# Kernel optimization log

Measured on AMD Instinct MI355X. Metric: run time of the kernel, lower is better.

Reference implementation:

```python
import jax, jax.numpy as jnp
import numpy as np

T, B, H = 512, 128, 512


def setup_inputs() -> dict:
    key = jax.random.key(0)
    k1, k2, k3 = jax.random.split(key, 3)
    x = jax.random.normal(k1, (T, B, H), dtype=jnp.float32)
    h0 = jnp.zeros((B, H), dtype=jnp.float32)
    # Orthogonal-ish scale via normal/sqrt(H) to keep gates in sane range
    Wi = jax.random.normal(k2, (H, 3 * H), dtype=jnp.float32) / np.sqrt(H)
    bi = jnp.zeros((3 * H,), dtype=jnp.float32)
    Wh = jax.random.normal(k3, (H, 3 * H), dtype=jnp.float32) / np.sqrt(H)
    bhn = jnp.zeros((H,), dtype=jnp.float32)
    return {"x": x, "h0": h0, "Wi": Wi, "bi": bi, "Wh": Wh, "bhn": bhn}


def reference(x, h0, Wi, bi, Wh, bhn):
    """GRU scanned over time, matching flax nn.GRUCell math.

    x: [T, B, H]; h0: [B, H]; Wi: [H, 3H] (r|z|n), bi: [3H];
    Wh: [H, 3H] (r|z|n, no bias except n-gate bhn: [H]).
    Returns (final_carry [B,H], outputs [T,B,H]).
    """
    hdim = h0.shape[-1]
    # Precompute all input projections in one big GEMM: [T, B, 3H]
    gi = jnp.einsum('tbh,hk->tbk', x, Wi) + bi

    def step(h, gi_t):
        gh = h @ Wh  # [B, 3H]
        gi_r, gi_z, gi_n = jnp.split(gi_t, 3, axis=-1)
        gh_r, gh_z, gh_n = jnp.split(gh, 3, axis=-1)
        r = jax.nn.sigmoid(gi_r + gh_r)
        z = jax.nn.sigmoid(gi_z + gh_z)
        n = jnp.tanh(gi_n + r * (gh_n + bhn))
        h_new = (1.0 - z) * n + z * h
        return h_new, h_new

    h_final, ys = jax.lax.scan(step, h0, gi)
    return h_final, ys
```

## Files before the change

kernel.cpp:

```cpp
#include <hip/hip_runtime.h>


#define TT 512
#define BB 128
#define HH 512
#define H3 1536
#define NWG 256
#define NTHR 1024

#define LDS_FLOATS 31232

__global__ __launch_bounds__(NTHR)
__attribute__((amdgpu_waves_per_eu(4, 4)))
void gru_scan(
    const float* __restrict__ x,
    const float* __restrict__ h0,
    const float* __restrict__ Wi,
    const float* __restrict__ bi,
    const float* __restrict__ Wh,
    const float* __restrict__ bhn,
    float* out,
    unsigned int* __restrict__ bars)
{
  __shared__ float lds[LDS_FLOATS];
  float*  Xs   = lds;
  float*  Hs   = lds + 8192;
  float4* red  = reinterpret_cast<float4*>(lds + 16384);
  float*  sums = lds + 29696;

  const int tid = threadIdx.x;
  const int n   = blockIdx.x;
  const int jt  = n & 31;
  const int bt  = n >> 5;
  const int j0  = jt * 16;
  const int b0  = bt * 16;

  const int w   = tid >> 6;
  const int kg  = (tid >> 4) & 3;
  const int jl  = tid & 15;
  const int kbase = (w & 7) * 64;
  const bool isH = (w < 8);

  unsigned int* grp = bars + bt * 32;

  float wa[48];
  {
    const float* __restrict__ W = isH ? Wh : Wi;
    #pragma unroll
    for (int m = 0; m < 4; ++m)
      #pragma unroll
      for (int kk = 0; kk < 4; ++kk) {
        const int k = kbase + m * 16 + kg * 4 + kk;
        #pragma unroll
        for (int g = 0; g < 3; ++g) {
          const float v = W[(size_t)k * H3 + g * HH + j0 + jl];
          asm volatile("v_accvgpr_write_b32 %0, %1"
                       : "=a"(wa[(m * 4 + kk) * 3 + g]) : "v"(v));
        }
      }
  }

  float* ys = out + BB * HH;

  float bir = 0.f, biz = 0.f, bin = 0.f, bhnv = 0.f;
  if (tid < 256) {
    const int jj = j0 + (tid & 15);
    bir  = bi[jj];
    biz  = bi[jj + HH];
    bin  = bi[jj + 2 * HH];
    bhnv = bhn[jj];
  }

  for (int t = 0; t < TT; ++t) {
    const float* __restrict__ xt = x + (size_t)t * BB * HH;
    const float* hp = t ? (ys + (size_t)(t - 1) * BB * HH) : h0;

    #pragma unroll
    for (int i = 0; i < 8; ++i) {
      const int idx = tid + i * NTHR;
      const int r = idx >> 9;
      const int c = idx & 511;
      Hs[r * 512 + c] = __hip_atomic_load(
          const_cast<float*>(hp) + (size_t)(b0 + r) * HH + c,
          __ATOMIC_RELAXED, __HIP_MEMORY_SCOPE_AGENT);
    }
    #pragma unroll
    for (int i = 0; i < 2; ++i) {
      const int idx = tid + i * NTHR;
      const int r = idx >> 7;
      const int c = idx & 127;
      const float4 xv = ((const float4*)(xt + (size_t)(b0 + r) * HH))[c];
      *(float4*)&Xs[r * 512 + c * 4] = xv;
    }
    __syncthreads();

    {
      const float* __restrict__ S = isH ? Hs : Xs;
      #pragma unroll
      for (int bq = 0; bq < 4; ++bq) {
        float a[4][3];
        #pragma unroll
        for (int r = 0; r < 4; ++r)
          #pragma unroll
          for (int g = 0; g < 3; ++g) a[r][g] = 0.f;

        #pragma unroll
        for (int m = 0; m < 4; ++m) {
          float wv[12];
          #pragma unroll
          for (int kk = 0; kk < 4; ++kk)
            #pragma unroll
            for (int g = 0; g < 3; ++g)
              asm volatile("v_accvgpr_read_b32 %0, %1"
                           : "=v"(wv[kk * 3 + g])
                           : "a"(wa[(m * 4 + kk) * 3 + g]));

          const float* Sm = S + kbase + m * 16 + kg * 4;
          const float4 v0 = *(const float4*)(Sm + (bq * 4 + 0) * 512);
          const float4 v1 = *(const float4*)(Sm + (bq * 4 + 1) * 512);
          const float4 v2 = *(const float4*)(Sm + (bq * 4 + 2) * 512);
          const float4 v3 = *(const float4*)(Sm + (bq * 4 + 3) * 512);
          #pragma unroll
          for (int g = 0; g < 3; ++g) {
            a[0][g] += v0.x*wv[0+g] + v0.y*wv[3+g] + v0.z*wv[6+g] + v0.w*wv[9+g];
            a[1][g] += v1.x*wv[0+g] + v1.y*wv[3+g] + v1.z*wv[6+g] + v1.w*wv[9+g];
            a[2][g] += v2.x*wv[0+g] + v2.y*wv[3+g] + v2.z*wv[6+g] + v2.w*wv[9+g];
            a[3][g] += v3.x*wv[0+g] + v3.y*wv[3+g] + v3.z*wv[6+g] + v3.w*wv[9+g];
          }
        }

        #pragma unroll
        for (int r = 0; r < 4; ++r)
          #pragma unroll
          for (int g = 0; g < 3; ++g) {
            a[r][g] += __shfl_xor(a[r][g], 16);
            a[r][g] += __shfl_xor(a[r][g], 32);
          }

        if (kg == bq) {
          float4* rp = red + (size_t)(w * 16 + jl) * 13 + bq * 3;
          #pragma unroll
          for (int g = 0; g < 3; ++g)
            rp[g] = make_float4(a[0][g], a[1][g], a[2][g], a[3][g]);
        }
      }
    }

    if (t + 1 < TT) {
      const float* xn = x + (size_t)(t + 1) * BB * HH;
      #pragma unroll
      for (int i = 0; i < 2; ++i) {
        const int idx = tid + i * NTHR;
        const int r = idx >> 7;
        const int c = idx & 127;
        const float4 v = ((const float4*)(xn + (size_t)(b0 + r) * HH))[c];
        asm volatile("" :: "v"(v.x), "v"(v.y), "v"(v.z), "v"(v.w));
      }
    }
    __syncthreads();

    {
      const int pm = tid >> 9;
      const int t9 = tid & 511;
      const int pjl = (t9 >> 4) & 15;
      const int pg  = (t9 >> 2) & 3;
      const int pbq = t9 & 3;
      if ((t9 & 256) == 0 && pg < 3) {
        float4 s = make_float4(0.f, 0.f, 0.f, 0.f);
        #pragma unroll
        for (int w2 = 0; w2 < 8; ++w2) {
          const float4 v = red[(size_t)(pm * 128 + w2 * 16 + pjl) * 13 + pbq * 3 + pg];
          s.x += v.x; s.y += v.y; s.z += v.z; s.w += v.w;
        }
        *(float4*)&sums[(size_t)(((pm * 16 + pjl) * 3) + pg) * 16 + pbq * 4] = s;
      }
    }
    __syncthreads();

    if (tid < 256) {
      const int eb  = tid >> 4;
      const int jl2 = tid & 15;
      const int jj  = j0 + jl2;
      const float ghr = sums[(jl2*3 + 0)*16 + eb];
      const float ghz = sums[(jl2*3 + 1)*16 + eb];
      const float ghn = sums[(jl2*3 + 2)*16 + eb];
      const float gir = sums[((16 + jl2)*3 + 0)*16 + eb];
      const float giz = sums[((16 + jl2)*3 + 1)*16 + eb];
      const float gin = sums[((16 + jl2)*3 + 2)*16 + eb];

      const float gr = gir + ghr + bir;
      const float gz = giz + ghz + biz;
      const float r  = 1.f / (1.f + __expf(-gr));
      const float z  = 1.f / (1.f + __expf(-gz));
      const float pre = gin + bin + r * (ghn + bhnv);
      const float e2 = __expf(2.f * pre);
      const float nn = 1.f - 2.f / (e2 + 1.f);
      const float hpv = Hs[eb * 512 + jj];
      const float h = (1.f - z) * nn + z * hpv;

      const size_t o = (size_t)(b0 + eb) * HH + jj;
      __hip_atomic_store(ys + (size_t)t * BB * HH + o, h,
                         __ATOMIC_RELAXED, __HIP_MEMORY_SCOPE_AGENT);
      if (t == TT - 1) out[o] = h;
    }

    if (t + 1 < TT) {
      __syncthreads();
      if (tid == 0) {
        __hip_atomic_fetch_add(grp, 1u, __ATOMIC_RELEASE,
                               __HIP_MEMORY_SCOPE_AGENT);
        const unsigned int target = 32u * (unsigned int)(t + 1);
        while (__hip_atomic_load(grp, __ATOMIC_RELAXED,
                                 __HIP_MEMORY_SCOPE_AGENT) < target)
          __builtin_amdgcn_s_sleep(1);
      }
      __syncthreads();
    }
  }
}

extern "C" void kernel_launch(void* const* d_in, const int* in_sizes, int n_in,
                              void* d_out, int out_size, void* d_ws, size_t ws_size,
                              hipStream_t stream) {
  const float* x   = (const float*)d_in[0];
  const float* h0  = (const float*)d_in[1];
  const float* Wi  = (const float*)d_in[2];
  const float* bi  = (const float*)d_in[3];
  const float* Wh  = (const float*)d_in[4];
  const float* bhn = (const float*)d_in[5];
  float* out = (float*)d_out;
  unsigned int* bars = (unsigned int*)d_ws;

  hipMemsetAsync(d_ws, 0, 8 * 128, stream);

  void* args[] = {(void*)&x, (void*)&h0, (void*)&Wi, (void*)&bi,
                  (void*)&Wh, (void*)&bhn, (void*)&out, (void*)&bars};
  hipLaunchCooperativeKernel(reinterpret_cast<const void*>(gru_scan),
                             dim3(NWG), dim3(NTHR), args, 0, stream);
}
```

Measured before the change: 15.74 ms.

## Split batch tile into two half-groups with separate barriers to overlap sync

```diff
diff --git a/kernel.cpp b/kernel.cpp
--- a/kernel.cpp
+++ b/kernel.cpp
@@ -8,7 +8,9 @@
 #define NWG 256
 #define NTHR 1024
 
-#define LDS_FLOATS 31232
+#define LDS_FLOATS 24320
+
+typedef float f32x4_t __attribute__((ext_vector_type(4)));
 
 __global__ __launch_bounds__(NTHR)
 __attribute__((amdgpu_waves_per_eu(4, 4)))
@@ -23,17 +25,20 @@
     unsigned int* __restrict__ bars)
 {
   __shared__ float lds[LDS_FLOATS];
-  float*  Xs   = lds;
-  float*  Hs   = lds + 8192;
+  float*  XsA  = lds;
+  float*  XsB  = lds + 4096;
+  float*  HsA  = lds + 8192;
+  float*  HsB  = lds + 12288;
   float4* red  = reinterpret_cast<float4*>(lds + 16384);
-  float*  sums = lds + 29696;
+  float*  sums = lds + 23552;
 
   const int tid = threadIdx.x;
   const int n   = blockIdx.x;
   const int jt  = n & 31;
-  const int bt  = n >> 5;
   const int j0  = jt * 16;
-  const int b0  = bt * 16;
+  const int btA = n >> 5;
+  const int b0A = btA * 8;
+  const int b0B = b0A + 64;
 
   const int w   = tid >> 6;
   const int kg  = (tid >> 4) & 3;
@@ -41,7 +46,8 @@
   const int kbase = (w & 7) * 64;
   const bool isH = (w < 8);
 
-  unsigned int* grp = bars + bt * 32;
+  unsigned int* grpA = bars + btA * 32;
+  unsigned int* grpB = bars + (btA + 8) * 32;
 
   float wa[48];
   {
@@ -63,7 +69,7 @@
   float* ys = out + BB * HH;
 
   float bir = 0.f, biz = 0.f, bin = 0.f, bhnv = 0.f;
-  if (tid < 256) {
+  if (tid < 128) {
     const int jj = j0 + (tid & 15);
     bir  = bi[jj];
     biz  = bi[jj + HH];
@@ -71,148 +77,163 @@
     bhnv = bhn[jj];
   }
 
+  {
+    const int r = tid >> 7;
+    const int c = tid & 127;
+    *(float4*)&XsA[r * 512 + c * 4] = ((const float4*)(x  + (size_t)(b0A + r) * HH))[c];
+    *(float4*)&XsB[r * 512 + c * 4] = ((const float4*)(x  + (size_t)(b0B + r) * HH))[c];
+    *(float4*)&HsA[r * 512 + c * 4] = ((const float4*)(h0 + (size_t)(b0A + r) * HH))[c];
+    *(float4*)&HsB[r * 512 + c * 4] = ((const float4*)(h0 + (size_t)(b0B + r) * HH))[c];
+  }
+  __syncthreads();
+
   for (int t = 0; t < TT; ++t) {
-    const float* __restrict__ xt = x + (size_t)t * BB * HH;
-    const float* hp = t ? (ys + (size_t)(t - 1) * BB * HH) : h0;
-
     #pragma unroll
-    for (int i = 0; i < 8; ++i) {
-      const int idx = tid + i * NTHR;
-      const int r = idx >> 9;
-      const int c = idx & 511;
-      Hs[r * 512 + c] = __hip_atomic_load(
-          const_cast<float*>(hp) + (size_t)(b0 + r) * HH + c,
-          __ATOMIC_RELAXED, __HIP_MEMORY_SCOPE_AGENT);
-    }
-    #pragma unroll
-    for (int i = 0; i < 2; ++i) {
-      const int idx = tid + i * NTHR;
-      const int r = idx >> 7;
-      const int c = idx & 127;
-      const float4 xv = ((const float4*)(xt + (size_t)(b0 + r) * HH))[c];
-      *(float4*)&Xs[r * 512 + c * 4] = xv;
-    }
-    __syncthreads();
-
-    {
-      const float* __restrict__ S = isH ? Hs : Xs;
-      #pragma unroll
-      for (int bq = 0; bq < 4; ++bq) {
-        float a[4][3];
+    for (int ph = 0; ph < 2; ++ph) {
+      const float* Hsx = ph ? HsB : HsA;
+      const float* Xsx = ph ? XsB : XsA;
+      const int    b0  = ph ? b0B : b0A;
+
+      {
+        const float* __restrict__ S = (isH ? Hsx : Xsx) + kbase;
         #pragma unroll
-        for (int r = 0; r < 4; ++r)
-          #pragma unroll
-          for (int g = 0; g < 3; ++g) a[r][g] = 0.f;
-
-        #pragma unroll
-        for (int m = 0; m < 4; ++m) {
-          float wv[12];
-          #pragma unroll
-          for (int kk = 0; kk < 4; ++kk)
+        for (int q = 0; q < 2; ++q) {
+          float a[4][3];
+          #pragma unroll
+          for (int r = 0; r < 4; ++r)
+            #pragma unroll
+            for (int g = 0; g < 3; ++g) a[r][g] = 0.f;
+
+          #pragma unroll
+          for (int m = 0; m < 4; ++m) {
+            float wv[12];
+            #pragma unroll
+            for (int kk = 0; kk < 4; ++kk)
+              #pragma unroll
+              for (int g = 0; g < 3; ++g)
+                asm volatile("v_accvgpr_read_b32 %0, %1"
+                             : "=v"(wv[kk * 3 + g])
+                             : "a"(wa[(m * 4 + kk) * 3 + g]));
+
+            const float* Sm = S + m * 16 + kg * 4;
+            const float4 v0 = *(const float4*)(Sm + (q * 4 + 0) * 512);
+            const float4 v1 = *(const float4*)(Sm + (q * 4 + 1) * 512);
+            const float4 v2 = *(const float4*)(Sm + (q * 4 + 2) * 512);
+            const float4 v3 = *(const float4*)(Sm + (q * 4 + 3) * 512);
+            #pragma unroll
+            for (int g = 0; g < 3; ++g) {
+              a[0][g] += v0.x*wv[0+g] + v0.y*wv[3+g] + v0.z*wv[6+g] + v0.w*wv[9+g];
+              a[1][g] += v1.x*wv[0+g] + v1.y*wv[3+g] + v1.z*wv[6+g] + v1.w*wv[9+g];
+              a[2][g] += v2.x*wv[0+g] + v2.y*wv[3+g] + v2.z*wv[6+g] + v2.w*wv[9+g];
+              a[3][g] += v3.x*wv[0+g] + v3.y*wv[3+g] + v3.z*wv[6+g] + v3.w*wv[9+g];
+            }
+          }
+
+          #pragma unroll
+          for (int r = 0; r < 4; ++r)
+            #pragma unroll
+            for (int g = 0; g < 3; ++g) {
+              a[r][g] += __shfl_xor(a[r][g], 16);
+              a[r][g] += __shfl_xor(a[r][g], 32);
+            }
+
+          if (kg == q) {
+            float4* rp = red + (size_t)(w * 16 + jl) * 7 + q * 3;
             #pragma unroll
             for (int g = 0; g < 3; ++g)
-              asm volatile("v_accvgpr_read_b32 %0, %1"
-                           : "=v"(wv[kk * 3 + g])
-                           : "a"(wa[(m * 4 + kk) * 3 + g]));
-
-          const float* Sm = S + kbase + m * 16 + kg * 4;
-          const float4 v0 = *(const float4*)(Sm + (bq * 4 + 0) * 512);
-          const float4 v1 = *(const float4*)(Sm + (bq * 4 + 1) * 512);
-          const float4 v2 = *(const float4*)(Sm + (bq * 4 + 2) * 512);
-          const float4 v3 = *(const float4*)(Sm + (bq * 4 + 3) * 512);
-          #pragma unroll
-          for (int g = 0; g < 3; ++g) {
-            a[0][g] += v0.x*wv[0+g] + v0.y*wv[3+g] + v0.z*wv[6+g] + v0.w*wv[9+g];
-            a[1][g] += v1.x*wv[0+g] + v1.y*wv[3+g] + v1.z*wv[6+g] + v1.w*wv[9+g];
-            a[2][g] += v2.x*wv[0+g] + v2.y*wv[3+g] + v2.z*wv[6+g] + v2.w*wv[9+g];
-            a[3][g] += v3.x*wv[0+g] + v3.y*wv[3+g] + v3.z*wv[6+g] + v3.w*wv[9+g];
+              rp[g] = make_float4(a[0][g], a[1][g], a[2][g], a[3][g]);
           }
         }
-
-        #pragma unroll
-        for (int r = 0; r < 4; ++r)
-          #pragma unroll
-          for (int g = 0; g < 3; ++g) {
-            a[r][g] += __shfl_xor(a[r][g], 16);
-            a[r][g] += __shfl_xor(a[r][g], 32);
+      }
+      __syncthreads();
+
+      if (tid < 256) {
+        const int pm  = tid >> 7;
+        const int pq  = (tid >> 6) & 1;
+        const int pg  = (tid >> 4) & 3;
+        const int pjl = tid & 15;
+        if (pg < 3) {
+          float4 s = make_float4(0.f, 0.f, 0.f, 0.f);
+          #pragma unroll
+          for (int w2 = 0; w2 < 8; ++w2) {
+            const float4 v = red[(size_t)((pm * 8 + w2) * 16 + pjl) * 7 + pq * 3 + pg];
+            s.x += v.x; s.y += v.y; s.z += v.z; s.w += v.w;
           }
-
-        if (kg == bq) {
-          float4* rp = red + (size_t)(w * 16 + jl) * 13 + bq * 3;
-          #pragma unroll
-          for (int g = 0; g < 3; ++g)
-            rp[g] = make_float4(a[0][g], a[1][g], a[2][g], a[3][g]);
+          *(float4*)&sums[(size_t)((pm * 16 + pjl) * 3 + pg) * 8 + pq * 4] = s;
         }
       }
+      __syncthreads();
+
+      if (tid < 128) {
+        const int eb  = tid >> 4;
+        const int jl2 = tid & 15;
+        const int jj  = j0 + jl2;
+        const float ghr = sums[((     jl2) * 3 + 0) * 8 + eb];
+        const float ghz = sums[((     jl2) * 3 + 1) * 8 + eb];
+        const float ghn = sums[((     jl2) * 3 + 2) * 8 + eb];
+        const float gir = sums[((16 + jl2) * 3 + 0) * 8 + eb];
+        const float giz = sums[((16 + jl2) * 3 + 1) * 8 + eb];
+        const float gin = sums[((16 + jl2) * 3 + 2) * 8 + eb];
+
+        const float gr = gir + ghr + bir;
+        const float gz = giz + ghz + biz;
+        const float r  = 1.f / (1.f + __expf(-gr));
+        const float z  = 1.f / (1.f + __expf(-gz));
+        const float pre = gin + bin + r * (ghn + bhnv);
+        const float e2 = __expf(2.f * pre);
+        const float nn = 1.f - 2.f / (e2 + 1.f);
+        const float hpv = Hsx[eb * 512 + jj];
+        const float h = (1.f - z) * nn + z * hpv;
+
+        const size_t o = (size_t)(b0 + eb) * HH + jj;
+        __hip_atomic_store(ys + (size_t)t * BB * HH + o, h,
+                           __ATOMIC_RELAXED, __HIP_MEMORY_SCOPE_AGENT);
+        if (t == TT - 1) out[o] = h;
+      }
+      __syncthreads();
+      if (tid == 0 && t + 1 < TT)
+        __hip_atomic_fetch_add(ph ? grpB : grpA, 1u, __ATOMIC_RELEASE,
+                               __HIP_MEMORY_SCOPE_AGENT);
     }
 
     if (t + 1 < TT) {
       const float* xn = x + (size_t)(t + 1) * BB * HH;
-      #pragma unroll
-      for (int i = 0; i < 2; ++i) {
-        const int idx = tid + i * NTHR;
-        const int r = idx >> 7;
-        const int c = idx & 127;
-        const float4 v = ((const float4*)(xn + (size_t)(b0 + r) * HH))[c];
-        asm volatile("" :: "v"(v.x), "v"(v.y), "v"(v.z), "v"(v.w));
-      }
-    }
-    __syncthreads();
-
-    {
-      const int pm = tid >> 9;
-      const int t9 = tid & 511;
-      const int pjl = (t9 >> 4) & 15;
-      const int pg  = (t9 >> 2) & 3;
-      const int pbq = t9 & 3;
-      if ((t9 & 256) == 0 && pg < 3) {
-        float4 s = make_float4(0.f, 0.f, 0.f, 0.f);
-        #pragma unroll
-        for (int w2 = 0; w2 < 8; ++w2) {
-          const float4 v = red[(size_t)(pm * 128 + w2 * 16 + pjl) * 13 + pbq * 3 + pg];
-          s.x += v.x; s.y += v.y; s.z += v.z; s.w += v.w;
-        }
-        *(float4*)&sums[(size_t)(((pm * 16 + pjl) * 3) + pg) * 16 + pbq * 4] = s;
-      }
-    }
-    __syncthreads();
-
-    if (tid < 256) {
-      const int eb  = tid >> 4;
-      const int jl2 = tid & 15;
-      const int jj  = j0 + jl2;
-      const float ghr = sums[(jl2*3 + 0)*16 + eb];
-      const float ghz = sums[(jl2*3 + 1)*16 + eb];
-      const float ghn = sums[(jl2*3 + 2)*16 + eb];
-      const float gir = sums[((16 + jl2)*3 + 0)*16 + eb];
-      const float giz = sums[((16 + jl2)*3 + 1)*16 + eb];
-      const float gin = sums[((16 + jl2)*3 + 2)*16 + eb];
-
-      const float gr = gir + ghr + bir;
-      const float gz = giz + ghz + biz;
-      const float r  = 1.f / (1.f + __expf(-gr));
-      const float z  = 1.f / (1.f + __expf(-gz));
-      const float pre = gin + bin + r * (ghn + bhnv);
-      const float e2 = __expf(2.f * pre);
-      const float nn = 1.f - 2.f / (e2 + 1.f);
-      const float hpv = Hs[eb * 512 + jj];
-      const float h = (1.f - z) * nn + z * hpv;
-
-      const size_t o = (size_t)(b0 + eb) * HH + jj;
-      __hip_atomic_store(ys + (size_t)t * BB * HH + o, h,
-                         __ATOMIC_RELAXED, __HIP_MEMORY_SCOPE_AGENT);
-      if (t == TT - 1) out[o] = h;
-    }
-
-    if (t + 1 < TT) {
-      __syncthreads();
+      const int r = tid >> 7;
+      const int c = tid & 127;
+      *(float4*)&XsA[r * 512 + c * 4] = ((const float4*)(xn + (size_t)(b0A + r) * HH))[c];
+      *(float4*)&XsB[r * 512 + c * 4] = ((const float4*)(xn + (size_t)(b0B + r) * HH))[c];
+
+      const unsigned int target = 32u * (unsigned int)(t + 1);
+      const float* ysrow = ys + (size_t)t * BB * HH;
+
       if (tid == 0) {
-        __hip_atomic_fetch_add(grp, 1u, __ATOMIC_RELEASE,
-                               __HIP_MEMORY_SCOPE_AGENT);
-        const unsigned int target = 32u * (unsigned int)(t + 1);
-        while (__hip_atomic_load(grp, __ATOMIC_RELAXED,
+        while (__hip_atomic_load(grpA, __ATOMIC_RELAXED,
                                  __HIP_MEMORY_SCOPE_AGENT) < target)
           __builtin_amdgcn_s_sleep(1);
+      }
+      __syncthreads();
+      {
+        const float* pa = ysrow + (size_t)(b0A + r) * HH + (c << 2);
+        f32x4_t hv;
+        asm volatile("global_load_dwordx4 %0, %1, off sc0 sc1\n\t"
+                     "s_waitcnt vmcnt(0)"
+                     : "=v"(hv) : "v"(pa) : "memory");
+        *(f32x4_t*)&HsA[r * 512 + c * 4] = hv;
+      }
+
+      if (tid == 0) {
+        while (__hip_atomic_load(grpB, __ATOMIC_RELAXED,
+                                 __HIP_MEMORY_SCOPE_AGENT) < target)
+          __builtin_amdgcn_s_sleep(1);
+      }
+      __syncthreads();
+      {
+        const float* pb = ysrow + (size_t)(b0B + r) * HH + (c << 2);
+        f32x4_t hv;
+        asm volatile("global_load_dwordx4 %0, %1, off sc0 sc1\n\t"
+                     "s_waitcnt vmcnt(0)"
+                     : "=v"(hv) : "v"(pb) : "memory");
+        *(f32x4_t*)&HsB[r * 512 + c * 4] = hv;
       }
       __syncthreads();
     }
@@ -231,7 +252,7 @@
   float* out = (float*)d_out;
   unsigned int* bars = (unsigned int*)d_ws;
 
-  hipMemsetAsync(d_ws, 0, 8 * 128, stream);
+  hipMemsetAsync(d_ws, 0, 16 * 128, stream);
 
   void* args[] = {(void*)&x, (void*)&h0, (void*)&Wi, (void*)&bi,
                   (void*)&Wh, (void*)&bhn, (void*)&out, (void*)&bars};
```

Result: slower. 18.17 ms (+15.5%).

## Overlap next-step input projection with recurrence and split barrier into per-wave waits

Applied to the files above, without the earlier changes.

```diff
diff --git a/kernel.cpp b/kernel.cpp
--- a/kernel.cpp
+++ b/kernel.cpp
@@ -8,7 +8,9 @@
 #define NWG 256
 #define NTHR 1024
 
-#define LDS_FLOATS 31232
+#define LDS_FLOATS 23040
+
+typedef float f32x4_t __attribute__((ext_vector_type(4)));
 
 __global__ __launch_bounds__(NTHR)
 __attribute__((amdgpu_waves_per_eu(4, 4)))
@@ -23,22 +25,24 @@
     unsigned int* __restrict__ bars)
 {
   __shared__ float lds[LDS_FLOATS];
-  float*  Xs   = lds;
-  float*  Hs   = lds + 8192;
-  float4* red  = reinterpret_cast<float4*>(lds + 16384);
-  float*  sums = lds + 29696;
-
-  const int tid = threadIdx.x;
-  const int n   = blockIdx.x;
-  const int jt  = n & 31;
-  const int bt  = n >> 5;
-  const int j0  = jt * 16;
-  const int b0  = bt * 16;
-
-  const int w   = tid >> 6;
-  const int kg  = (tid >> 4) & 3;
-  const int jl  = tid & 15;
-  const int kbase = (w & 7) * 64;
+  float*  Hs  = lds;
+  float4* red = (float4*)(lds + 8192);
+  float*  gif = lds + 21504;
+  float4* gi4 = (float4*)gif;
+
+  const int tid  = threadIdx.x;
+  const int n    = blockIdx.x;
+  const int jt   = n & 31;
+  const int bt   = n >> 5;
+  const int j0   = jt * 16;
+  const int b0   = bt * 16;
+
+  const int w    = tid >> 6;
+  const int lane = tid & 63;
+  const int kg   = (tid >> 4) & 3;
+  const int jl   = tid & 15;
+  const int wh   = w & 7;
+  const int kbase = wh * 64;
   const bool isH = (w < 8);
 
   unsigned int* grp = bars + bt * 32;
@@ -71,39 +75,106 @@
     bhnv = bhn[jj];
   }
 
+  if (isH) {
+    #pragma unroll
+    for (int i = 0; i < 4; ++i) {
+      const int flat = i * 64 + lane;
+      const int r = flat >> 4, cf4 = flat & 15;
+      *(float4*)&Hs[wh * 1024 + flat * 4] =
+          *(const float4*)(h0 + (size_t)(b0 + r) * HH + kbase + cf4 * 4);
+    }
+  } else {
+    #pragma unroll
+    for (int q = 0; q < 4; ++q) {
+      float a[4][3];
+      #pragma unroll
+      for (int r = 0; r < 4; ++r)
+        #pragma unroll
+        for (int g = 0; g < 3; ++g) a[r][g] = 0.f;
+      #pragma unroll
+      for (int m = 0; m < 4; ++m) {
+        float wv[12];
+        #pragma unroll
+        for (int kk = 0; kk < 4; ++kk)
+          #pragma unroll
+          for (int g = 0; g < 3; ++g)
+            asm volatile("v_accvgpr_read_b32 %0, %1"
+                         : "=v"(wv[kk * 3 + g]) : "a"(wa[(m * 4 + kk) * 3 + g]));
+        const float* P = x + (size_t)(b0 + q * 4) * HH + kbase + m * 16 + kg * 4;
+        const float4 v0 = *(const float4*)(P);
+        const float4 v1 = *(const float4*)(P + HH);
+        const float4 v2 = *(const float4*)(P + 2 * HH);
+        const float4 v3 = *(const float4*)(P + 3 * HH);
+        #pragma unroll
+        for (int g = 0; g < 3; ++g) {
+          a[0][g] += v0.x*wv[0+g] + v0.y*wv[3+g] + v0.z*wv[6+g] + v0.w*wv[9+g];
+          a[1][g] += v1.x*wv[0+g] + v1.y*wv[3+g] + v1.z*wv[6+g] + v1.w*wv[9+g];
+          a[2][g] += v2.x*wv[0+g] + v2.y*wv[3+g] + v2.z*wv[6+g] + v2.w*wv[9+g];
+          a[3][g] += v3.x*wv[0+g] + v3.y*wv[3+g] + v3.z*wv[6+g] + v3.w*wv[9+g];
+        }
+      }
+      #pragma unroll
+      for (int r = 0; r < 4; ++r)
+        #pragma unroll
+        for (int g = 0; g < 3; ++g) {
+          a[r][g] += __shfl_xor(a[r][g], 16);
+          a[r][g] += __shfl_xor(a[r][g], 32);
+        }
+      if (kg == q) {
+        float4* rp = red + (size_t)(w * 16 + jl) * 13 + q * 3;
+        #pragma unroll
+        for (int g = 0; g < 3; ++g)
+          rp[g] = make_float4(a[0][g], a[1][g], a[2][g], a[3][g]);
+      }
+    }
+  }
+  __syncthreads();
+  if (tid >= 512 && tid < 768) {
+    const int t9  = tid - 512;
+    const int pjl = t9 >> 4;
+    const int pg  = (t9 >> 2) & 3;
+    const int pbq = t9 & 3;
+    if (pg < 3) {
+      float4 s = make_float4(0.f, 0.f, 0.f, 0.f);
+      #pragma unroll
+      for (int w2 = 0; w2 < 8; ++w2) {
+        const float4 v = red[(size_t)((8 + w2) * 16 + pjl) * 13 + pbq * 3 + pg];
+        s.x += v.x; s.y += v.y; s.z += v.z; s.w += v.w;
+      }
+      gi4[(pbq * 3 + pg) * 16 + pjl] = s;
+    }
+  }
+  __syncthreads();
+
   for (int t = 0; t < TT; ++t) {
-    const float* __restrict__ xt = x + (size_t)t * BB * HH;
-    const float* hp = t ? (ys + (size_t)(t - 1) * BB * HH) : h0;
-
-    #pragma unroll
-    for (int i = 0; i < 8; ++i) {
-      const int idx = tid + i * NTHR;
-      const int r = idx >> 9;
-      const int c = idx & 511;
-      Hs[r * 512 + c] = __hip_atomic_load(
-          const_cast<float*>(hp) + (size_t)(b0 + r) * HH + c,
-          __ATOMIC_RELAXED, __HIP_MEMORY_SCOPE_AGENT);
-    }
-    #pragma unroll
-    for (int i = 0; i < 2; ++i) {
-      const int idx = tid + i * NTHR;
-      const int r = idx >> 7;
-      const int c = idx & 127;
-      const float4 xv = ((const float4*)(xt + (size_t)(b0 + r) * HH))[c];
-      *(float4*)&Xs[r * 512 + c * 4] = xv;
-    }
-    __syncthreads();
-
-    {
-      const float* __restrict__ S = isH ? Hs : Xs;
-      #pragma unroll
-      for (int bq = 0; bq < 4; ++bq) {
+    if (isH) {
+      if (t > 0) {
+        if (lane == 0) {
+          const unsigned int target = 32u * (unsigned int)t;
+          while (__hip_atomic_load(grp, __ATOMIC_RELAXED,
+                                   __HIP_MEMORY_SCOPE_AGENT) < target)
+            __builtin_amdgcn_s_sleep(2);
+        }
+        const float* src = ys + (size_t)(t - 1) * BB * HH;
+        #pragma unroll
+        for (int i = 0; i < 4; ++i) {
+          const int flat = i * 64 + lane;
+          const int r = flat >> 4, cf4 = flat & 15;
+          const float* p = src + (size_t)(b0 + r) * HH + kbase + cf4 * 4;
+          f32x4_t hv;
+          asm volatile("global_load_dwordx4 %0, %1, off sc0 sc1"
+                       : "=v"(hv) : "v"(p));
+          *(f32x4_t*)&Hs[wh * 1024 + flat * 4] = hv;
+        }
+      }
+      const float* S = Hs + wh * 1024;
+      #pragma unroll
+      for (int q = 0; q < 4; ++q) {
         float a[4][3];
         #pragma unroll
         for (int r = 0; r < 4; ++r)
           #pragma unroll
           for (int g = 0; g < 3; ++g) a[r][g] = 0.f;
-
         #pragma unroll
         for (int m = 0; m < 4; ++m) {
           float wv[12];
@@ -112,14 +183,12 @@
             #pragma unroll
             for (int g = 0; g < 3; ++g)
               asm volatile("v_accvgpr_read_b32 %0, %1"
-                           : "=v"(wv[kk * 3 + g])
-                           : "a"(wa[(m * 4 + kk) * 3 + g]));
-
-          const float* Sm = S + kbase + m * 16 + kg * 4;
-          const float4 v0 = *(const float4*)(Sm + (bq * 4 + 0) * 512);
-          const float4 v1 = *(const float4*)(Sm + (bq * 4 + 1) * 512);
-          const float4 v2 = *(const float4*)(Sm + (bq * 4 + 2) * 512);
-          const float4 v3 = *(const float4*)(Sm + (bq * 4 + 3) * 512);
+                           : "=v"(wv[kk * 3 + g]) : "a"(wa[(m * 4 + kk) * 3 + g]));
+          const int cb = (m * 4 + kg) * 4;
+          const float4 v0 = *(const float4*)&S[(q * 4 + 0) * 64 + cb];
+          const float4 v1 = *(const float4*)&S[(q * 4 + 1) * 64 + cb];
+          const float4 v2 = *(const float4*)&S[(q * 4 + 2) * 64 + cb];
+          const float4 v3 = *(const float4*)&S[(q * 4 + 3) * 64 + cb];
           #pragma unroll
           for (int g = 0; g < 3; ++g) {
             a[0][g] += v0.x*wv[0+g] + v0.y*wv[3+g] + v0.z*wv[6+g] + v0.w*wv[9+g];
@@ -128,7 +197,6 @@
             a[3][g] += v3.x*wv[0+g] + v3.y*wv[3+g] + v3.z*wv[6+g] + v3.w*wv[9+g];
           }
         }
-
         #pragma unroll
         for (int r = 0; r < 4; ++r)
           #pragma unroll
@@ -136,43 +204,57 @@
             a[r][g] += __shfl_xor(a[r][g], 16);
             a[r][g] += __shfl_xor(a[r][g], 32);
           }
-
-        if (kg == bq) {
-          float4* rp = red + (size_t)(w * 16 + jl) * 13 + bq * 3;
+        if (kg == q) {
+          float4* rp = red + (size_t)(w * 16 + jl) * 13 + q * 3;
           #pragma unroll
           for (int g = 0; g < 3; ++g)
             rp[g] = make_float4(a[0][g], a[1][g], a[2][g], a[3][g]);
         }
       }
-    }
-
-    if (t + 1 < TT) {
-      const float* xn = x + (size_t)(t + 1) * BB * HH;
-      #pragma unroll
-      for (int i = 0; i < 2; ++i) {
-        const int idx = tid + i * NTHR;
-        const int r = idx >> 7;
-        const int c = idx & 127;
-        const float4 v = ((const float4*)(xn + (size_t)(b0 + r) * HH))[c];
-        asm volatile("" :: "v"(v.x), "v"(v.y), "v"(v.z), "v"(v.w));
-      }
-    }
-    __syncthreads();
-
-    {
-      const int pm = tid >> 9;
-      const int t9 = tid & 511;
-      const int pjl = (t9 >> 4) & 15;
-      const int pg  = (t9 >> 2) & 3;
-      const int pbq = t9 & 3;
-      if ((t9 & 256) == 0 && pg < 3) {
-        float4 s = make_float4(0.f, 0.f, 0.f, 0.f);
-        #pragma unroll
-        for (int w2 = 0; w2 < 8; ++w2) {
-          const float4 v = red[(size_t)(pm * 128 + w2 * 16 + pjl) * 13 + pbq * 3 + pg];
-          s.x += v.x; s.y += v.y; s.z += v.z; s.w += v.w;
-        }
-        *(float4*)&sums[(size_t)(((pm * 16 + pjl) * 3) + pg) * 16 + pbq * 4] = s;
+    } else if (t + 1 < TT) {
+      const float* xt1 = x + (size_t)(t + 1) * BB * HH;
+      #pragma unroll
+      for (int q = 0; q < 4; ++q) {
+        float a[4][3];
+        #pragma unroll
+        for (int r = 0; r < 4; ++r)
+          #pragma unroll
+          for (int g = 0; g < 3; ++g) a[r][g] = 0.f;
+        #pragma unroll
+        for (int m = 0; m < 4; ++m) {
+          float wv[12];
+          #pragma unroll
+          for (int kk = 0; kk < 4; ++kk)
+            #pragma unroll
+            for (int g = 0; g < 3; ++g)
+              asm volatile("v_accvgpr_read_b32 %0, %1"
+                           : "=v"(wv[kk * 3 + g]) : "a"(wa[(m * 4 + kk) * 3 + g]));
+          const float* P = xt1 + (size_t)(b0 + q * 4) * HH + kbase + m * 16 + kg * 4;
+          const float4 v0 = *(const float4*)(P);
+          const float4 v1 = *(const float4*)(P + HH);
+          const float4 v2 = *(const float4*)(P + 2 * HH);
+          const float4 v3 = *(const float4*)(P + 3 * HH);
+          #pragma unroll
+          for (int g = 0; g < 3; ++g) {
+            a[0][g] += v0.x*wv[0+g] + v0.y*wv[3+g] + v0.z*wv[6+g] + v0.w*wv[9+g];
+            a[1][g] += v1.x*wv[0+g] + v1.y*wv[3+g] + v1.z*wv[6+g] + v1.w*wv[9+g];
+            a[2][g] += v2.x*wv[0+g] + v2.y*wv[3+g] + v2.z*wv[6+g] + v2.w*wv[9+g];
+            a[3][g] += v3.x*wv[0+g] + v3.y*wv[3+g] + v3.z*wv[6+g] + v3.w*wv[9+g];
+          }
+        }
+        #pragma unroll
+        for (int r = 0; r < 4; ++r)
+          #pragma unroll
+          for (int g = 0; g < 3; ++g) {
+            a[r][g] += __shfl_xor(a[r][g], 16);
+            a[r][g] += __shfl_xor(a[r][g], 32);
+          }
+        if (kg == q) {
+          float4* rp = red + (size_t)(w * 16 + jl) * 13 + q * 3;
+          #pragma unroll
+          for (int g = 0; g < 3; ++g)
+            rp[g] = make_float4(a[0][g], a[1][g], a[2][g], a[3][g]);
+        }
       }
     }
     __syncthreads();
@@ -181,12 +263,20 @@
       const int eb  = tid >> 4;
       const int jl2 = tid & 15;
       const int jj  = j0 + jl2;
-      const float ghr = sums[(jl2*3 + 0)*16 + eb];
-      const float ghz = sums[(jl2*3 + 1)*16 + eb];
-      const float ghn = sums[(jl2*3 + 2)*16 + eb];
-      const float gir = sums[((16 + jl2)*3 + 0)*16 + eb];
-      const float giz = sums[((16 + jl2)*3 + 1)*16 + eb];
-      const float gin = sums[((16 + jl2)*3 + 2)*16 + eb];
+      const int c   = eb & 3;
+      const int bq3 = (eb >> 2) * 3;
+      float ghr = 0.f, ghz = 0.f, ghn = 0.f;
+      #pragma unroll
+      for (int w2 = 0; w2 < 8; ++w2) {
+        const float* rp = (const float*)&red[(size_t)(w2 * 16 + jl2) * 13 + bq3];
+        ghr += rp[c];
+        ghz += rp[4 + c];
+        ghn += rp[8 + c];
+      }
+      const int p = (t & 1) * 768;
+      const float gir = gif[p + (bq3 + 0) * 64 + jl2 * 4 + c];
+      const float giz = gif[p + (bq3 + 1) * 64 + jl2 * 4 + c];
+      const float gin = gif[p + (bq3 + 2) * 64 + jl2 * 4 + c];
 
       const float gr = gir + ghr + bir;
       const float gz = giz + ghz + biz;
@@ -195,27 +285,33 @@
       const float pre = gin + bin + r * (ghn + bhnv);
       const float e2 = __expf(2.f * pre);
       const float nn = 1.f - 2.f / (e2 + 1.f);
-      const float hpv = Hs[eb * 512 + jj];
+      const float hpv = Hs[(jj >> 6) * 1024 + eb * 64 + (jj & 63)];
       const float h = (1.f - z) * nn + z * hpv;
 
       const size_t o = (size_t)(b0 + eb) * HH + jj;
       __hip_atomic_store(ys + (size_t)t * BB * HH + o, h,
                          __ATOMIC_RELAXED, __HIP_MEMORY_SCOPE_AGENT);
       if (t == TT - 1) out[o] = h;
-    }
-
-    if (t + 1 < TT) {
-      __syncthreads();
-      if (tid == 0) {
-        __hip_atomic_fetch_add(grp, 1u, __ATOMIC_RELEASE,
-                               __HIP_MEMORY_SCOPE_AGENT);
-        const unsigned int target = 32u * (unsigned int)(t + 1);
-        while (__hip_atomic_load(grp, __ATOMIC_RELAXED,
-                                 __HIP_MEMORY_SCOPE_AGENT) < target)
-          __builtin_amdgcn_s_sleep(1);
-      }
-      __syncthreads();
-    }
+    } else if (tid >= 512 && tid < 768 && t + 1 < TT) {
+      const int t9  = tid - 512;
+      const int pjl = t9 >> 4;
+      const int pg  = (t9 >> 2) & 3;
+      const int pbq = t9 & 3;
+      if (pg < 3) {
+        float4 s = make_float4(0.f, 0.f, 0.f, 0.f);
+        #pragma unroll
+        for (int w2 = 0; w2 < 8; ++w2) {
+          const float4 v = red[(size_t)((8 + w2) * 16 + pjl) * 13 + pbq * 3 + pg];
+          s.x += v.x; s.y += v.y; s.z += v.z; s.w += v.w;
+        }
+        gi4[((t + 1) & 1) * 192 + (pbq * 3 + pg) * 16 + pjl] = s;
+      }
+    }
+    __syncthreads();
+
+    if (tid == 0 && t + 1 < TT)
+      __hip_atomic_fetch_add(grp, 1u, __ATOMIC_RELAXED,
+                             __HIP_MEMORY_SCOPE_AGENT);
   }
 }
 
```

Result: faster. 14.02 ms (-10.9%).
